# Kernel tuning notes

Hardware: AMD Instinct MI355X
Metric: run time of the kernel (lower is better)

## Reference

```python
import jax, jax.numpy as jnp
import numpy as np

B, T, C = 4, 2048, 1024
H, D = 16, 64  # n_head, head_dim; H*D == C
EPS = 1e-12


def _l2norm(x):
    # matches torch F.normalize(dim=-1): x / max(||x||_2, eps)
    n = jnp.sqrt(jnp.sum(x * x, axis=-1, keepdims=True))
    return x / jnp.maximum(n, EPS)


def setup_inputs() -> dict:
    key = jax.random.key(0)
    ks = jax.random.split(key, 8)
    s = 0.02
    return {
        "x": jax.random.normal(ks[0], (B, T, C), dtype=jnp.float32),
        "Wq": jax.random.normal(ks[1], (C, C), dtype=jnp.float32) * s,
        "Wk": jax.random.normal(ks[2], (C, C), dtype=jnp.float32) * s,
        "Wv": jax.random.normal(ks[3], (C, C), dtype=jnp.float32) * s,
        "Wbeta": jax.random.normal(ks[4], (H, C), dtype=jnp.float32) * s,
        "bbeta": jnp.zeros((H,), dtype=jnp.float32),
        "Wgate": jax.random.normal(ks[5], (C, C), dtype=jnp.float32) * s,
        "Wo": jax.random.normal(ks[6], (C, C), dtype=jnp.float32) * s,
    }


def _forward(x, Wq, Wk, Wv, Wbeta, bbeta, Wgate, Wo):
    q = (x @ Wq.T).reshape(B, T, H, D)
    k = (x @ Wk.T).reshape(B, T, H, D)
    v = (x @ Wv.T).reshape(B, T, H, D)
    beta = jax.nn.sigmoid(x @ Wbeta.T + bbeta)  # (B,T,H)
    gate = jax.nn.sigmoid(x @ Wgate.T)          # (B,T,C)

    q = _l2norm(q)
    k = _l2norm(k)

    # time-major for scan: (T,B,H,D) / (T,B,H)
    qT = jnp.transpose(q, (1, 0, 2, 3))
    kT = jnp.transpose(k, (1, 0, 2, 3))
    vT = jnp.transpose(v, (1, 0, 2, 3))
    bT = jnp.transpose(beta, (1, 0, 2))

    M0 = jnp.zeros((B, H, D, D), dtype=x.dtype)

    def step(M, inp):
        q_t, k_t, v_t, b_t = inp
        o_t = jnp.einsum('bhdc,bhc->bhd', M, q_t)       # read state with q (pre-update)
        Mk = jnp.einsum('bhdc,bhc->bhd', M, k_t)
        dv = v_t - Mk                                    # delta-rule error
        M = M + b_t[..., None, None] * jnp.einsum('bhd,bhc->bhdc', dv, k_t)
        return M, o_t

    _, oT = jax.lax.scan(step, M0, (qT, kT, vT, bT))     # oT: (T,B,H,D)
    o = jnp.transpose(oT, (1, 0, 2, 3)).reshape(B, T, C)
    return (gate * o) @ Wo.T


def reference(x, Wq, Wk, Wv, Wbeta, bbeta, Wgate, Wo):
    return _forward(x, Wq, Wk, Wv, Wbeta, bbeta, Wgate, Wo)
```

## Files before the change

### kernel.cpp

```cpp
#include <hip/hip_runtime.h>
#include <cstdint>
#include <cstddef>

#define Bz 4
#define Tz 2048
#define Cz 1024
#define Hz 16
#define Dz 64
#define NTOK (Bz*Tz)
#define CHL 32
#define NCH (Tz/CHL)

typedef __attribute__((ext_vector_type(8))) short  short8;
typedef __attribute__((ext_vector_type(4))) float  floatx4;

__device__ __forceinline__ unsigned short f2bf(float x) {
  union { float f; uint32_t u; } a; a.f = x;
  uint32_t r = a.u + 0x7fffu + ((a.u >> 16) & 1u);
  return (unsigned short)(r >> 16);
}
__device__ __forceinline__ float bf2f(unsigned short u) {
  union { uint32_t i; float f; } a; a.i = ((uint32_t)u) << 16; return a.f;
}
__device__ __forceinline__ float sigmoidf_(float z) {
  return 1.0f / (1.0f + __expf(-z));
}
__device__ __forceinline__ uint32_t cvtpk_bf16(float a, float b) {
  uint32_t d;
  asm volatile("v_cvt_pk_bf16_f32 %0, %1, %2" : "=v"(d) : "v"(a), "v"(b));
  return d;
}
__device__ __forceinline__ float lo16f(uint32_t u) {
  union { uint32_t i; float f; } a; a.i = u << 16; return a.f;
}
__device__ __forceinline__ float hi16f(uint32_t u) {
  union { uint32_t i; float f; } a; a.i = u & 0xffff0000u; return a.f;
}

__device__ __forceinline__ void gload_lds16(const void* gptr, void* lptr) {
  __builtin_amdgcn_global_load_lds(
      (const __attribute__((address_space(1))) void*)(uintptr_t)gptr,
      (__attribute__((address_space(3))) void*)(uint32_t)(uintptr_t)lptr,
      16, 0, 0);
}

template<int CTRL>
__device__ __forceinline__ float dpp_addf(float x) {
  int y = __builtin_amdgcn_update_dpp(0, __float_as_int(x), CTRL, 0xF, 0xF, true);
  return x + __int_as_float(y);
}
__device__ __forceinline__ float rowsum16(float x) {
  x = dpp_addf<0xB1>(x);
  x = dpp_addf<0x4E>(x);
  x = dpp_addf<0x124>(x);
  x = dpp_addf<0x128>(x);
  return x;
}

union FragU { uint32_t u[4]; short8 s; };

__global__ __launch_bounds__(256) void cvt6_kernel(
    const float* __restrict__ s0, const float* __restrict__ s1,
    const float* __restrict__ s2, const float* __restrict__ s3,
    const float* __restrict__ s4, const float* __restrict__ s5,
    unsigned short* __restrict__ d0, unsigned short* __restrict__ d1,
    unsigned short* __restrict__ d2, unsigned short* __restrict__ d3,
    unsigned short* __restrict__ d4, unsigned short* __restrict__ d5,
    int n4x, int n4w)
{
  const int w = blockIdx.y;
  const float* s = (w == 0) ? s0 : (w == 1) ? s1 : (w == 2) ? s2 : (w == 3) ? s3 : (w == 4) ? s4 : s5;
  unsigned short* d = (w == 0) ? d0 : (w == 1) ? d1 : (w == 2) ? d2 : (w == 3) ? d3 : (w == 4) ? d4 : d5;
  const int n4 = (w == 0) ? n4x : n4w;
  int i = blockIdx.x * blockDim.x + threadIdx.x;
  int stride = gridDim.x * blockDim.x;
  const float4* in4 = (const float4*)s;
  ushort4* out4 = (ushort4*)d;
  for (; i < n4; i += stride) {
    float4 f = in4[i];
    ushort4 u;
    u.x = f2bf(f.x); u.y = f2bf(f.y); u.z = f2bf(f.z); u.w = f2bf(f.w);
    out4[i] = u;
  }
}

#define VM8()  asm volatile("s_waitcnt vmcnt(8)" ::: "memory")
#define VM6()  asm volatile("s_waitcnt vmcnt(6)" ::: "memory")
#define VM4()  asm volatile("s_waitcnt vmcnt(4)" ::: "memory")
#define VM3()  asm volatile("s_waitcnt vmcnt(3)" ::: "memory")
#define VM0()  asm volatile("s_waitcnt vmcnt(0)" ::: "memory")
#define LGKM0() asm volatile("s_waitcnt lgkmcnt(0)" ::: "memory")
#define BARR() __builtin_amdgcn_s_barrier()

template<int BN, int OB16>
__global__ __launch_bounds__(512, 2) void gemm256_kernel(
    const unsigned short* __restrict__ A,
    const unsigned short* __restrict__ W0, const unsigned short* __restrict__ W1,
    const unsigned short* __restrict__ W2, const unsigned short* __restrict__ W3,
    void* __restrict__ O0, void* __restrict__ O1,
    void* __restrict__ O2, void* __restrict__ O3,
    int M, int N, int K, int nz_sigmoid, int norm_mask)
{
  constexpr int LB  = (BN == 256) ? 2 : 1;
  constexpr int NJ  = BN / 64;
  constexpr int AH  = 8192;
  constexpr int BH  = BN * 32;
  constexpr int PAR = 2 * AH + 2 * BH;
  __shared__ unsigned short smem[2 * PAR];

  const int gx = gridDim.x, gz = gridDim.z;
  const int nwg = gx * gridDim.y * gz;
  int flat = (blockIdx.z * gridDim.y + blockIdx.y) * gx + blockIdx.x;
  if ((nwg & 7) == 0) flat = (flat & 7) * (nwg >> 3) + (flat >> 3);
  const int xz = gx * gz;
  const int by = flat / xz;
  const int rem = flat - by * xz;
  const int bz = rem / gx;
  const int bx = rem - bz * gx;

  const unsigned short* Bw = (bz == 0) ? W0 : (bz == 1) ? W1 : (bz == 2) ? W2 : W3;
  void* Cw = (bz == 0) ? O0 : (bz == 1) ? O1 : (bz == 2) ? O2 : O3;
  const bool act = (bz == nz_sigmoid);
  const bool donorm = (norm_mask >> bz) & 1;

  const int m0 = by * 256, n0 = bx * BN;
  const int tid = threadIdx.x;
  const int wid = tid >> 6, lane = tid & 63;
  const int wm = wid >> 2, wn = wid & 3;
  const int ml = lane & 15, kq = lane >> 4;

  const unsigned short* Ap = A  + (size_t)m0 * K;
  const unsigned short* Bp = Bw + (size_t)n0 * K;

  const int srow = wid * 16 + (lane >> 2);
  const int ss8  = ((lane & 3) ^ ((lane >> 3) & 3)) * 8;
  const int rs8  = (kq ^ ((ml >> 1) & 3)) * 8;
  const int arow = wm * 128 + ml;
  const int brow = wn * (BN / 4) + ml;

  const int NT = K >> 6;
  const int hmax = NT << 2;

  floatx4 acc[8][NJ];
#pragma unroll
  for (int i = 0; i < 8; ++i)
#pragma unroll
    for (int j = 0; j < NJ; ++j) acc[i][j] = floatx4{0.f, 0.f, 0.f, 0.f};

#define HOFF(hh) ((hh) == 0 ? 0 : (hh) == 1 ? AH : (hh) == 2 ? AH + BH : 2 * AH + BH)
#define STAGE1(hsi) do {                                                      \
    const int ht_ = (hsi) >> 2, hh_ = (hsi) & 3;                              \
    const bool isB_ = hh_ & 1;                                                \
    const unsigned short* p_ = isB_ ? Bp : Ap;                                \
    const int kb_ = ht_ * 64 + (hh_ >> 1) * 32;                               \
    unsigned short* lb_ = &smem[(ht_ & 1) * PAR + HOFF(hh_) + wid * 512];     \
    gload_lds16(p_ + (size_t)srow * K + kb_ + ss8, lb_);                      \
    if (!isB_ || LB == 2)                                                     \
      gload_lds16(p_ + (size_t)(128 + srow) * K + kb_ + ss8, lb_ + 4096);     \
  } while (0)

  int hs = 0;
  for (; hs < 6 && hs < hmax; ++hs) STAGE1(hs);
  if constexpr (BN == 256) { VM8(); } else { VM6(); }
  BARR();

#define LOAD_A(Hb, mh)                                                        \
  _Pragma("unroll") for (int i = 0; i < 4; ++i)                               \
    af[i] = *(const short8*)&Hb[(arow + (mh) * 64 + i * 16) * 32 + rs8];
#define LOAD_B(Hb)                                                            \
  _Pragma("unroll") for (int j = 0; j < NJ; ++j)                              \
    bf[j] = *(const short8*)&Hb[(brow + j * 16) * 32 + rs8];
#define MFMA_Q(mh)                                                            \
  __builtin_amdgcn_s_setprio(1);                                              \
  _Pragma("unroll") for (int i = 0; i < 4; ++i)                               \
    _Pragma("unroll") for (int j = 0; j < NJ; ++j)                            \
      acc[(mh) * 4 + i][j] = __builtin_amdgcn_mfma_f32_16x16x32_bf16(         \
          af[i], bf[j], acc[(mh) * 4 + i][j], 0, 0, 0);                       \
  __builtin_amdgcn_s_setprio(0);
#define STAGE_NEXT() do { if (hs < hmax) { STAGE1(hs); ++hs; } } while (0)

  short8 af[4], bf[NJ];
  for (int t = 0; t < NT; ++t) {
    const unsigned short* Ah0 = &smem[(t & 1) * PAR + HOFF(0)];
    const unsigned short* Bh0 = &smem[(t & 1) * PAR + HOFF(1)];
    const unsigned short* Ah1 = &smem[(t & 1) * PAR + HOFF(2)];
    const unsigned short* Bh1 = &smem[(t & 1) * PAR + HOFF(3)];

    LOAD_A(Ah0, 0); LOAD_B(Bh0);
    STAGE_NEXT();
    BARR(); LGKM0();
    MFMA_Q(0);
    BARR();

    LOAD_A(Ah0, 1);
    STAGE_NEXT();
    BARR(); LGKM0();
    MFMA_Q(1);
    if (t == NT - 1) { VM0(); }
    else { if constexpr (BN == 256) { VM8(); } else { VM6(); } }
    BARR();

    LOAD_A(Ah1, 0); LOAD_B(Bh1);
    STAGE_NEXT();
    BARR(); LGKM0();
    MFMA_Q(0);
    BARR();

    LOAD_A(Ah1, 1);
    STAGE_NEXT();
    BARR(); LGKM0();
    MFMA_Q(1);
    if (t < NT - 2) { if constexpr (BN == 256) { VM8(); } else { VM6(); } }
    else if (t == NT - 2) { if constexpr (BN == 256) { VM4(); } else { VM3(); } }
    BARR();
  }

  float scale[8][4];
  if (donorm) {
#pragma unroll
    for (int i = 0; i < 8; ++i) {
#pragma unroll
      for (int r = 0; r < 4; ++r) {
        float ss = 0.f;
#pragma unroll
        for (int j = 0; j < NJ; ++j) ss = fmaf(acc[i][j][r], acc[i][j][r], ss);
        ss = rowsum16(ss);
        scale[i][r] = 1.0f / fmaxf(sqrtf(ss), 1e-12f);
      }
    }
  }

  const int row_base = m0 + wm * 128;
  const int col_base = n0 + wn * (BN / 4);
#pragma unroll
  for (int i = 0; i < 8; ++i) {
#pragma unroll
    for (int j = 0; j < NJ; ++j) {
      const int col = col_base + j * 16 + ml;
#pragma unroll
      for (int r = 0; r < 4; ++r) {
        const int row = row_base + i * 16 + kq * 4 + r;
        float val = acc[i][j][r];
        if (donorm) val *= scale[i][r];
        if (act) val = sigmoidf_(val);
        if constexpr (OB16) ((unsigned short*)Cw)[(size_t)row * N + col] = f2bf(val);
        else                ((float*)Cw)[(size_t)row * N + col] = val;
      }
    }
  }
}

__global__ __launch_bounds__(256) void beta_kernel(
    const float* __restrict__ x, const float* __restrict__ Wb,
    const float* __restrict__ bb, float* __restrict__ beta_out)
{
  const int n = blockIdx.x;
  const int wid = threadIdx.x >> 6;
  const int lane = threadIdx.x & 63;
  const float* xr = x + (size_t)n * Cz;
  for (int h = wid; h < Hz; h += 4) {
    const float* wr = Wb + (size_t)h * Cz;
    float s = 0.f;
#pragma unroll 4
    for (int i = lane; i < Cz; i += 64) s = fmaf(xr[i], wr[i], s);
#pragma unroll
    for (int ofs = 32; ofs >= 1; ofs >>= 1) s += __shfl_xor(s, ofs);
    if (lane == 0) beta_out[(size_t)n * Hz + h] = sigmoidf_(s + bb[h]);
  }
}

__global__ __launch_bounds__(256) void deltachunk_phase1(
    const unsigned short* __restrict__ qb, const unsigned short* __restrict__ kb,
    const unsigned short* __restrict__ vb, const float* __restrict__ betaf,
    float* __restrict__ of,
    unsigned short* __restrict__ qtb, unsigned short* __restrict__ wbuf,
    unsigned short* __restrict__ ubuf, unsigned short* __restrict__ ktb)
{
  __shared__ unsigned short Kb[32][72], Qb[32][72], Vb[32][72];
  __shared__ float As[32][36];
  __shared__ unsigned short Sb[32][40];
  __shared__ unsigned short Us[32][72], Ws[32][72], Qts[32][72];
  __shared__ float bsh[32];

  const int bid = blockIdx.x;
  const int chain = bid & 63;
  const int chunk = bid >> 6;
  const int b = chain >> 4, h = chain & 15;
  const int tid = threadIdx.x;
  const int wid = tid >> 6, lane = tid & 63;
  const int ml = lane & 15, kq = lane >> 4;

  const size_t tok0 = (size_t)b * Tz + (size_t)chunk * CHL;
  const size_t cb = ((size_t)chain * NCH + chunk) * 2048;

  {
    const int row = tid >> 3, c8 = (tid & 7) * 8;
    const size_t ga = (tok0 + row) * Cz + h * Dz + c8;
    *(uint4*)&Qb[row][c8] = *(const uint4*)&qb[ga];
    *(uint4*)&Kb[row][c8] = *(const uint4*)&kb[ga];
    *(uint4*)&Vb[row][c8] = *(const uint4*)&vb[ga];
  }
  if (tid < 32) bsh[tid] = betaf[(tok0 + tid) * Hz + h];
  __syncthreads();

  {
    const int tr = wid & 1, tc = wid >> 1;
    floatx4 accA = {0.f,0.f,0.f,0.f}, accS = {0.f,0.f,0.f,0.f};
#pragma unroll
    for (int eh = 0; eh < 2; ++eh) {
      short8 ka = *(const short8*)&Kb[tr * 16 + ml][eh * 32 + kq * 8];
      short8 kbf = *(const short8*)&Kb[tc * 16 + ml][eh * 32 + kq * 8];
      short8 qa = *(const short8*)&Qb[tr * 16 + ml][eh * 32 + kq * 8];
      accA = __builtin_amdgcn_mfma_f32_16x16x32_bf16(ka, kbf, accA, 0, 0, 0);
      accS = __builtin_amdgcn_mfma_f32_16x16x32_bf16(qa, kbf, accS, 0, 0, 0);
    }
#pragma unroll
    for (int r = 0; r < 4; ++r) {
      int t = tr * 16 + kq * 4 + r;
      int s = tc * 16 + ml;
      As[s][t] = bsh[t] * accA[r];
      Sb[t][s] = (t > s) ? f2bf(accS[r]) : (unsigned short)0;
    }
  }
  __syncthreads();

  if (tid < 128) {
    const int j = tid;
    float x[32];
    if (j < 64) {
#pragma unroll
      for (int t = 0; t < 32; ++t) x[t] = bsh[t] * bf2f(Vb[t][j]);
    } else {
#pragma unroll
      for (int t = 0; t < 32; ++t) x[t] = bsh[t] * bf2f(Kb[t][j - 64]);
    }
#pragma unroll
    for (int t = 0; t < 31; ++t) {
      float xt = x[t];
#pragma unroll
      for (int s = t + 1; s < 32; ++s) x[s] = fmaf(-As[t][s], xt, x[s]);
    }
    if (j < 64) {
#pragma unroll
      for (int t = 0; t < 32; ++t) Us[t][j] = f2bf(x[t]);
    } else {
#pragma unroll
      for (int t = 0; t < 32; ++t) Ws[t][j - 64] = f2bf(x[t]);
    }
  }
  __syncthreads();

  {
    const int dw = wid * 16 + ml;
    FragU bu, bw;
#pragma unroll
    for (int r = 0; r < 4; ++r) {
      bu.u[r] = (uint32_t)Us[kq * 8 + 2 * r][dw] | ((uint32_t)Us[kq * 8 + 2 * r + 1][dw] << 16);
      bw.u[r] = (uint32_t)Ws[kq * 8 + 2 * r][dw] | ((uint32_t)Ws[kq * 8 + 2 * r + 1][dw] << 16);
    }
    floatx4 accO[2], accQ[2];
#pragma unroll
    for (int tt = 0; tt < 2; ++tt) { accO[tt] = floatx4{0.f,0.f,0.f,0.f}; accQ[tt] = floatx4{0.f,0.f,0.f,0.f}; }
#pragma unroll
    for (int tt = 0; tt < 2; ++tt) {
      short8 sa = *(const short8*)&Sb[tt * 16 + ml][kq * 8];
      accO[tt] = __builtin_amdgcn_mfma_f32_16x16x32_bf16(sa, bu.s, accO[tt], 0, 0, 0);
      accQ[tt] = __builtin_amdgcn_mfma_f32_16x16x32_bf16(sa, bw.s, accQ[tt], 0, 0, 0);
    }
#pragma unroll
    for (int tt = 0; tt < 2; ++tt) {
#pragma unroll
      for (int r = 0; r < 4; ++r) {
        int t = tt * 16 + kq * 4 + r;
        of[(tok0 + t) * Cz + h * Dz + dw] = accO[tt][r];
        Qts[t][dw] = f2bf(bf2f(Qb[t][dw]) - accQ[tt][r]);
      }
    }
  }

  unsigned short ktmp[8], utmp[8];
  {
    const int e = tid >> 2, tq = (tid & 3) * 8;
#pragma unroll
    for (int i2 = 0; i2 < 8; ++i2) { ktmp[i2] = Kb[tq + i2][e]; utmp[i2] = Us[tq + i2][e]; }
  }
  __syncthreads();

  {
    const int row = tid >> 3, c8 = (tid & 7) * 8;
    const size_t o16 = cb + (size_t)row * 64 + c8;
    *(uint4*)&qtb[o16]  = *(const uint4*)&Qts[row][c8];
    *(uint4*)&wbuf[o16] = *(const uint4*)&Ws[row][c8];
    const int e = tid >> 2, tq = (tid & 3) * 8;
    *(uint4*)&ktb[cb + (size_t)e * 32 + tq]  = *(const uint4*)ktmp;
    *(uint4*)&ubuf[cb + (size_t)e * 32 + tq] = *(const uint4*)utmp;
  }
}

__global__ __launch_bounds__(256) void deltachunk_phase2(
    const unsigned short* __restrict__ qtb, const unsigned short* __restrict__ wbuf,
    const unsigned short* __restrict__ ubuf, const unsigned short* __restrict__ ktb,
    const unsigned short* __restrict__ gbuf, const float* __restrict__ ofv,
    unsigned short* __restrict__ ab)
{
  __shared__ unsigned short Gb[2][64][72];
  __shared__ unsigned short Ub[2][32][40];
  __shared__ unsigned short Kts[2][64][40];
  __shared__ unsigned short Mh[2][32][72], Ml[2][32][72];

  const int chain = blockIdx.x >> 1;
  const int dh = blockIdx.x & 1;
  const int b = chain >> 4, h = chain & 15;
  const int d0 = dh * 32;
  const int tid = threadIdx.x;
  const int wid = tid >> 6, lane = tid & 63;
  const int ml = lane & 15, kq = lane >> 4;
  const int iq = wid >> 1, jq = wid & 1;

  const size_t cbase = (size_t)chain * NCH * 2048;
  const int gcol = h * Dz + d0 + jq * 16 + ml;

  const int grow = tid >> 2;
  const int gc16 = (tid & 3) * 16;
  const int ke   = tid >> 2;
  const int kc8  = (tid & 3) * 8;
  const int ue   = tid >> 3;
  const int uc4  = (tid & 7) * 4;

  const unsigned short* gsrc = (grow < 32) ? qtb : wbuf;
  const size_t gsoff = (size_t)(grow & 31) * 64 + gc16;

  unsigned short pg[8]; float pf[8];
  {
    *(uint4*)&Gb[0][grow][gc16]     = *(const uint4*)&gsrc[cbase + gsoff];
    *(uint4*)&Gb[0][grow][gc16 + 8] = *(const uint4*)&gsrc[cbase + gsoff + 8];
    *(uint4*)&Kts[0][ke][kc8]       = *(const uint4*)&ktb[cbase + (size_t)ke * 32 + kc8];
    *(uint2*)&Ub[0][ue][uc4]        = *(const uint2*)&ubuf[cbase + (size_t)(d0 + ue) * 32 + uc4];
  }
  if (iq == 0) {
    const size_t t0 = (size_t)b * Tz;
#pragma unroll
    for (int ti = 0; ti < 2; ++ti)
#pragma unroll
      for (int r = 0; r < 4; ++r) {
        const size_t gi = (t0 + ti * 16 + kq * 4 + r) * Cz + gcol;
        pg[ti * 4 + r] = gbuf[gi];
        pf[ti * 4 + r] = ofv[gi];
      }
  }
  for (int i = tid; i < 32 * 72; i += 256) { (&Mh[0][0][0])[i] = 0; (&Ml[0][0][0])[i] = 0; }
  __syncthreads();

  const int idxA = (ml + 16 * ((kq & 1) * 2)) * 4;
  const int idxB = (ml + 16 * ((kq & 1) * 2 + 1)) * 4;
  const bool hiKq = (kq >= 2);

  floatx4 mAcc[4];
#pragma unroll
  for (int a = 0; a < 4; ++a) mAcc[a] = floatx4{0.f, 0.f, 0.f, 0.f};

  for (int c = 0; c < NCH; ++c) {
    const int cbuf = c & 1, nbuf = cbuf ^ 1;
    const int mr = c & 1, mw = mr ^ 1;
    const size_t tok0 = (size_t)b * Tz + (size_t)c * CHL;

    const int cn = (c + 1 < NCH) ? c + 1 : c;
    const size_t cbn = cbase + (size_t)cn * 2048;
    uint4 sg0 = *(const uint4*)&gsrc[cbn + gsoff];
    uint4 sg1 = *(const uint4*)&gsrc[cbn + gsoff + 8];
    uint4 sk  = *(const uint4*)&ktb[cbn + (size_t)ke * 32 + kc8];
    uint2 su  = *(const uint2*)&ubuf[cbn + (size_t)(d0 + ue) * 32 + uc4];
    unsigned short ng[8]; float nf[8];
    if (iq == 0) {
      const size_t tkn = (size_t)b * Tz + (size_t)cn * CHL;
#pragma unroll
      for (int ti = 0; ti < 2; ++ti)
#pragma unroll
        for (int r = 0; r < 4; ++r) {
          const size_t gi = (tkn + ti * 16 + kq * 4 + r) * Cz + gcol;
          ng[ti * 4 + r] = gbuf[gi];
          nf[ti * 4 + r] = ofv[gi];
        }
    }

    floatx4 g1[2];
    g1[0] = floatx4{0.f,0.f,0.f,0.f}; g1[1] = floatx4{0.f,0.f,0.f,0.f};
#pragma unroll
    for (int eh = 0; eh < 2; ++eh) {
      short8 afr0 = *(const short8*)&Gb[cbuf][iq * 32 + 0  + ml][eh * 32 + kq * 8];
      short8 afr1 = *(const short8*)&Gb[cbuf][iq * 32 + 16 + ml][eh * 32 + kq * 8];
      short8 bh = *(const short8*)&Mh[mr][jq * 16 + ml][eh * 32 + kq * 8];
      short8 bl = *(const short8*)&Ml[mr][jq * 16 + ml][eh * 32 + kq * 8];
      g1[0] = __builtin_amdgcn_mfma_f32_16x16x32_bf16(afr0, bh, g1[0], 0, 0, 0);
      g1[0] = __builtin_amdgcn_mfma_f32_16x16x32_bf16(afr0, bl, g1[0], 0, 0, 0);
      g1[1] = __builtin_amdgcn_mfma_f32_16x16x32_bf16(afr1, bh, g1[1], 0, 0, 0);
      g1[1] = __builtin_amdgcn_mfma_f32_16x16x32_bf16(afr1, bl, g1[1], 0, 0, 0);
    }

    if (iq == 0) {
#pragma unroll
      for (int ti = 0; ti < 2; ++ti)
#pragma unroll
        for (int r = 0; r < 4; ++r) {
          const size_t gi = (tok0 + ti * 16 + kq * 4 + r) * Cz + gcol;
          const float val = bf2f(pg[ti * 4 + r]) * (pf[ti * 4 + r] + g1[ti][r]);
          ab[gi] = f2bf(val);
        }
#pragma unroll
      for (int e = 0; e < 8; ++e) { pg[e] = ng[e]; pf[e] = nf[e]; }
    } else {
      uint32_t pkh[2][2], pkl[2][2];
#pragma unroll
      for (int ti = 0; ti < 2; ++ti) {
        ushort4 uu = *(const ushort4*)&Ub[cbuf][jq * 16 + ml][ti * 16 + kq * 4];
        float z0 = bf2f(uu.x) - g1[ti][0];
        float z1 = bf2f(uu.y) - g1[ti][1];
        float z2 = bf2f(uu.z) - g1[ti][2];
        float z3 = bf2f(uu.w) - g1[ti][3];
        uint32_t h01 = cvtpk_bf16(z0, z1), h23 = cvtpk_bf16(z2, z3);
        pkh[ti][0] = h01; pkh[ti][1] = h23;
        pkl[ti][0] = cvtpk_bf16(z0 - lo16f(h01), z1 - hi16f(h01));
        pkl[ti][1] = cvtpk_bf16(z2 - lo16f(h23), z3 - hi16f(h23));
      }
      FragU zh, zl;
#pragma unroll
      for (int s = 0; s < 4; ++s) {
        const int idx = (s < 2) ? idxA : idxB;
        const int rp = s & 1;
        int v0 = __builtin_amdgcn_ds_bpermute(idx, (int)pkh[0][rp]);
        int v1 = __builtin_amdgcn_ds_bpermute(idx, (int)pkh[1][rp]);
        zh.u[s] = hiKq ? (uint32_t)v1 : (uint32_t)v0;
        int w0 = __builtin_amdgcn_ds_bpermute(idx, (int)pkl[0][rp]);
        int w1 = __builtin_amdgcn_ds_bpermute(idx, (int)pkl[1][rp]);
        zl.u[s] = hiKq ? (uint32_t)w1 : (uint32_t)w0;
      }
#pragma unroll
      for (int et = 0; et < 4; ++et) {
        short8 kfr = *(const short8*)&Kts[cbuf][et * 16 + ml][kq * 8];
        mAcc[et] = __builtin_amdgcn_mfma_f32_16x16x32_bf16(kfr, zh.s, mAcc[et], 0, 0, 0);
        mAcc[et] = __builtin_amdgcn_mfma_f32_16x16x32_bf16(kfr, zl.s, mAcc[et], 0, 0, 0);
      }
#pragma unroll
      for (int et = 0; et < 4; ++et) {
        float m0 = mAcc[et][0], m1 = mAcc[et][1], m2 = mAcc[et][2], m3 = mAcc[et][3];
        uint32_t h01 = cvtpk_bf16(m0, m1), h23 = cvtpk_bf16(m2, m3);
        uint32_t l01 = cvtpk_bf16(m0 - lo16f(h01), m1 - hi16f(h01));
        uint32_t l23 = cvtpk_bf16(m2 - lo16f(h23), m3 - hi16f(h23));
        *(uint2*)&Mh[mw][jq * 16 + ml][et * 16 + kq * 4] = make_uint2(h01, h23);
        *(uint2*)&Ml[mw][jq * 16 + ml][et * 16 + kq * 4] = make_uint2(l01, l23);
      }
    }

    *(uint4*)&Gb[nbuf][grow][gc16]     = sg0;
    *(uint4*)&Gb[nbuf][grow][gc16 + 8] = sg1;
    *(uint4*)&Kts[nbuf][ke][kc8]       = sk;
    *(uint2*)&Ub[nbuf][ue][uc4]        = su;

    LGKM0();
    BARR();
  }
}

extern "C" void kernel_launch(void* const* d_in, const int* in_sizes, int n_in,
                              void* d_out, int out_size, void* d_ws, size_t ws_size,
                              hipStream_t stream) {
  const float* x     = (const float*)d_in[0];
  const float* Wq    = (const float*)d_in[1];
  const float* Wk    = (const float*)d_in[2];
  const float* Wv    = (const float*)d_in[3];
  const float* Wbeta = (const float*)d_in[4];
  const float* bbeta = (const float*)d_in[5];
  const float* Wgate = (const float*)d_in[6];
  const float* Wo    = (const float*)d_in[7];
  float* out = (float*)d_out;

  char* ws = (char*)d_ws;
  size_t off = 0;
  auto alloc = [&](size_t bytes) -> char* {
    char* p = ws + off;
    off += (bytes + 255) & ~(size_t)255;
    return p;
  };
  unsigned short* xb  = (unsigned short*)alloc((size_t)NTOK * Cz * 2);
  unsigned short* Wqb = (unsigned short*)alloc((size_t)Cz * Cz * 2);
  unsigned short* Wkb = (unsigned short*)alloc((size_t)Cz * Cz * 2);
  unsigned short* Wvb = (unsigned short*)alloc((size_t)Cz * Cz * 2);
  unsigned short* Wgb = (unsigned short*)alloc((size_t)Cz * Cz * 2);
  unsigned short* Wob = (unsigned short*)alloc((size_t)Cz * Cz * 2);
  unsigned short* qb  = (unsigned short*)alloc((size_t)NTOK * Cz * 2);
  unsigned short* kb  = (unsigned short*)alloc((size_t)NTOK * Cz * 2);
  unsigned short* vb  = (unsigned short*)alloc((size_t)NTOK * Cz * 2);
  unsigned short* gb  = (unsigned short*)alloc((size_t)NTOK * Cz * 2);
  float* of    = (float*)alloc((size_t)NTOK * Cz * 4);
  float* betaf = (float*)alloc((size_t)NTOK * Hz * 4);
  unsigned short* qtb  = (unsigned short*)alloc((size_t)64 * NCH * 2048 * 2);
  unsigned short* wbuf = (unsigned short*)alloc((size_t)64 * NCH * 2048 * 2);
  unsigned short* ubuf = (unsigned short*)alloc((size_t)64 * NCH * 2048 * 2);
  unsigned short* ktb  = (unsigned short*)alloc((size_t)64 * NCH * 2048 * 2);
  unsigned short* ab = xb;

  const int n4x = NTOK * Cz / 4;
  const int n4w = Cz * Cz / 4;

  cvt6_kernel<<<dim3(1024, 6), dim3(256), 0, stream>>>(
      x, Wq, Wk, Wv, Wgate, Wo, xb, Wqb, Wkb, Wvb, Wgb, Wob, n4x, n4w);

  gemm256_kernel<256, 1><<<dim3(Cz / 256, NTOK / 256, 4), dim3(512), 0, stream>>>(
      xb, Wqb, Wkb, Wvb, Wgb, qb, kb, vb, gb, NTOK, Cz, Cz, 3, 3);

  beta_kernel<<<dim3(NTOK), dim3(256), 0, stream>>>(x, Wbeta, bbeta, betaf);

  deltachunk_phase1<<<dim3(64 * NCH), dim3(256), 0, stream>>>(
      qb, kb, vb, betaf, of, qtb, wbuf, ubuf, ktb);

  deltachunk_phase2<<<dim3(128), dim3(256), 0, stream>>>(
      qtb, wbuf, ubuf, ktb, gb, of, ab);

  gemm256_kernel<128, 0><<<dim3(Cz / 128, NTOK / 256, 1), dim3(512), 0, stream>>>(
      ab, Wob, Wob, Wob, Wob, out, out, out, out, NTOK, Cz, Cz, -1, 0);
}
```

Before: 366.9 us.

## Fuse x bf16 conversion into beta kernel and merge phase2 halves per block

```diff
diff --git a/kernel.cpp b/kernel.cpp
--- a/kernel.cpp
+++ b/kernel.cpp
@@ -59,28 +59,23 @@
 
 union FragU { uint32_t u[4]; short8 s; };
 
-__global__ __launch_bounds__(256) void cvt6_kernel(
+__global__ __launch_bounds__(256) void cvt5_kernel(
     const float* __restrict__ s0, const float* __restrict__ s1,
     const float* __restrict__ s2, const float* __restrict__ s3,
-    const float* __restrict__ s4, const float* __restrict__ s5,
+    const float* __restrict__ s4,
     unsigned short* __restrict__ d0, unsigned short* __restrict__ d1,
     unsigned short* __restrict__ d2, unsigned short* __restrict__ d3,
-    unsigned short* __restrict__ d4, unsigned short* __restrict__ d5,
-    int n4x, int n4w)
+    unsigned short* __restrict__ d4, int n4)
 {
   const int w = blockIdx.y;
-  const float* s = (w == 0) ? s0 : (w == 1) ? s1 : (w == 2) ? s2 : (w == 3) ? s3 : (w == 4) ? s4 : s5;
-  unsigned short* d = (w == 0) ? d0 : (w == 1) ? d1 : (w == 2) ? d2 : (w == 3) ? d3 : (w == 4) ? d4 : d5;
-  const int n4 = (w == 0) ? n4x : n4w;
+  const float* s = (w == 0) ? s0 : (w == 1) ? s1 : (w == 2) ? s2 : (w == 3) ? s3 : s4;
+  unsigned short* d = (w == 0) ? d0 : (w == 1) ? d1 : (w == 2) ? d2 : (w == 3) ? d3 : d4;
   int i = blockIdx.x * blockDim.x + threadIdx.x;
-  int stride = gridDim.x * blockDim.x;
-  const float4* in4 = (const float4*)s;
-  ushort4* out4 = (ushort4*)d;
-  for (; i < n4; i += stride) {
-    float4 f = in4[i];
+  if (i < n4) {
+    float4 f = ((const float4*)s)[i];
     ushort4 u;
     u.x = f2bf(f.x); u.y = f2bf(f.y); u.z = f2bf(f.z); u.w = f2bf(f.w);
-    out4[i] = u;
+    ((ushort4*)d)[i] = u;
   }
 }
 
@@ -252,12 +247,19 @@
 
 __global__ __launch_bounds__(256) void beta_kernel(
     const float* __restrict__ x, const float* __restrict__ Wb,
-    const float* __restrict__ bb, float* __restrict__ beta_out)
+    const float* __restrict__ bb, float* __restrict__ beta_out,
+    unsigned short* __restrict__ xb16)
 {
   const int n = blockIdx.x;
   const int wid = threadIdx.x >> 6;
   const int lane = threadIdx.x & 63;
   const float* xr = x + (size_t)n * Cz;
+  {
+    float4 f = ((const float4*)xr)[threadIdx.x];
+    ushort4 u;
+    u.x = f2bf(f.x); u.y = f2bf(f.y); u.z = f2bf(f.z); u.w = f2bf(f.w);
+    ((ushort4*)(xb16 + (size_t)n * Cz))[threadIdx.x] = u;
+  }
   for (int h = wid; h < Hz; h += 4) {
     const float* wr = Wb + (size_t)h * Cz;
     float s = 0.f;
@@ -397,45 +399,41 @@
   }
 }
 
-__global__ __launch_bounds__(256) void deltachunk_phase2(
+__global__ __launch_bounds__(512) void deltachunk_phase2(
     const unsigned short* __restrict__ qtb, const unsigned short* __restrict__ wbuf,
     const unsigned short* __restrict__ ubuf, const unsigned short* __restrict__ ktb,
     const unsigned short* __restrict__ gbuf, const float* __restrict__ ofv,
     unsigned short* __restrict__ ab)
 {
   __shared__ unsigned short Gb[2][64][72];
-  __shared__ unsigned short Ub[2][32][40];
+  __shared__ unsigned short Ub[2][64][40];
   __shared__ unsigned short Kts[2][64][40];
-  __shared__ unsigned short Mh[2][32][72], Ml[2][32][72];
-
-  const int chain = blockIdx.x >> 1;
-  const int dh = blockIdx.x & 1;
+  __shared__ unsigned short Mh[2][2][32][72], Ml[2][2][32][72];
+
+  const int chain = blockIdx.x;
   const int b = chain >> 4, h = chain & 15;
-  const int d0 = dh * 32;
   const int tid = threadIdx.x;
   const int wid = tid >> 6, lane = tid & 63;
   const int ml = lane & 15, kq = lane >> 4;
-  const int iq = wid >> 1, jq = wid & 1;
+  const int dh = wid >> 2;
+  const int iq = (wid >> 1) & 1, jq = wid & 1;
+  const int d0 = dh * 32;
 
   const size_t cbase = (size_t)chain * NCH * 2048;
   const int gcol = h * Dz + d0 + jq * 16 + ml;
 
-  const int grow = tid >> 2;
-  const int gc16 = (tid & 3) * 16;
-  const int ke   = tid >> 2;
-  const int kc8  = (tid & 3) * 8;
-  const int ue   = tid >> 3;
-  const int uc4  = (tid & 7) * 4;
+  const int grow = tid >> 3, gc8 = (tid & 7) * 8;
+  const int ke   = tid >> 3, kc4 = (tid & 7) * 4;
+  const int ue   = tid >> 3, uc4 = (tid & 7) * 4;
 
   const unsigned short* gsrc = (grow < 32) ? qtb : wbuf;
-  const size_t gsoff = (size_t)(grow & 31) * 64 + gc16;
+  const size_t gsoff = (size_t)(grow & 31) * 64 + gc8;
 
   unsigned short pg[8]; float pf[8];
   {
-    *(uint4*)&Gb[0][grow][gc16]     = *(const uint4*)&gsrc[cbase + gsoff];
-    *(uint4*)&Gb[0][grow][gc16 + 8] = *(const uint4*)&gsrc[cbase + gsoff + 8];
-    *(uint4*)&Kts[0][ke][kc8]       = *(const uint4*)&ktb[cbase + (size_t)ke * 32 + kc8];
-    *(uint2*)&Ub[0][ue][uc4]        = *(const uint2*)&ubuf[cbase + (size_t)(d0 + ue) * 32 + uc4];
+    *(uint4*)&Gb[0][grow][gc8] = *(const uint4*)&gsrc[cbase + gsoff];
+    *(uint2*)&Kts[0][ke][kc4]  = *(const uint2*)&ktb[cbase + (size_t)ke * 32 + kc4];
+    *(uint2*)&Ub[0][ue][uc4]   = *(const uint2*)&ubuf[cbase + (size_t)ue * 32 + uc4];
   }
   if (iq == 0) {
     const size_t t0 = (size_t)b * Tz;
@@ -448,7 +446,7 @@
         pf[ti * 4 + r] = ofv[gi];
       }
   }
-  for (int i = tid; i < 32 * 72; i += 256) { (&Mh[0][0][0])[i] = 0; (&Ml[0][0][0])[i] = 0; }
+  for (int i = tid; i < 2 * 32 * 72; i += 512) { (&Mh[0][0][0][0])[i] = 0; (&Ml[0][0][0][0])[i] = 0; }
   __syncthreads();
 
   const int idxA = (ml + 16 * ((kq & 1) * 2)) * 4;
@@ -466,10 +464,9 @@
 
     const int cn = (c + 1 < NCH) ? c + 1 : c;
     const size_t cbn = cbase + (size_t)cn * 2048;
-    uint4 sg0 = *(const uint4*)&gsrc[cbn + gsoff];
-    uint4 sg1 = *(const uint4*)&gsrc[cbn + gsoff + 8];
-    uint4 sk  = *(const uint4*)&ktb[cbn + (size_t)ke * 32 + kc8];
-    uint2 su  = *(const uint2*)&ubuf[cbn + (size_t)(d0 + ue) * 32 + uc4];
+    uint4 sg = *(const uint4*)&gsrc[cbn + gsoff];
+    uint2 sk = *(const uint2*)&ktb[cbn + (size_t)ke * 32 + kc4];
+    uint2 su = *(const uint2*)&ubuf[cbn + (size_t)ue * 32 + uc4];
     unsigned short ng[8]; float nf[8];
     if (iq == 0) {
       const size_t tkn = (size_t)b * Tz + (size_t)cn * CHL;
@@ -489,8 +486,8 @@
     for (int eh = 0; eh < 2; ++eh) {
       short8 afr0 = *(const short8*)&Gb[cbuf][iq * 32 + 0  + ml][eh * 32 + kq * 8];
       short8 afr1 = *(const short8*)&Gb[cbuf][iq * 32 + 16 + ml][eh * 32 + kq * 8];
-      short8 bh = *(const short8*)&Mh[mr][jq * 16 + ml][eh * 32 + kq * 8];
-      short8 bl = *(const short8*)&Ml[mr][jq * 16 + ml][eh * 32 + kq * 8];
+      short8 bh = *(const short8*)&Mh[mr][dh][jq * 16 + ml][eh * 32 + kq * 8];
+      short8 bl = *(const short8*)&Ml[mr][dh][jq * 16 + ml][eh * 32 + kq * 8];
       g1[0] = __builtin_amdgcn_mfma_f32_16x16x32_bf16(afr0, bh, g1[0], 0, 0, 0);
       g1[0] = __builtin_amdgcn_mfma_f32_16x16x32_bf16(afr0, bl, g1[0], 0, 0, 0);
       g1[1] = __builtin_amdgcn_mfma_f32_16x16x32_bf16(afr1, bh, g1[1], 0, 0, 0);
@@ -512,7 +509,7 @@
       uint32_t pkh[2][2], pkl[2][2];
 #pragma unroll
       for (int ti = 0; ti < 2; ++ti) {
-        ushort4 uu = *(const ushort4*)&Ub[cbuf][jq * 16 + ml][ti * 16 + kq * 4];
+        ushort4 uu = *(const ushort4*)&Ub[cbuf][d0 + jq * 16 + ml][ti * 16 + kq * 4];
         float z0 = bf2f(uu.x) - g1[ti][0];
         float z1 = bf2f(uu.y) - g1[ti][1];
         float z2 = bf2f(uu.z) - g1[ti][2];
@@ -546,15 +543,14 @@
         uint32_t h01 = cvtpk_bf16(m0, m1), h23 = cvtpk_bf16(m2, m3);
         uint32_t l01 = cvtpk_bf16(m0 - lo16f(h01), m1 - hi16f(h01));
         uint32_t l23 = cvtpk_bf16(m2 - lo16f(h23), m3 - hi16f(h23));
-        *(uint2*)&Mh[mw][jq * 16 + ml][et * 16 + kq * 4] = make_uint2(h01, h23);
-        *(uint2*)&Ml[mw][jq * 16 + ml][et * 16 + kq * 4] = make_uint2(l01, l23);
-      }
-    }
-
-    *(uint4*)&Gb[nbuf][grow][gc16]     = sg0;
-    *(uint4*)&Gb[nbuf][grow][gc16 + 8] = sg1;
-    *(uint4*)&Kts[nbuf][ke][kc8]       = sk;
-    *(uint2*)&Ub[nbuf][ue][uc4]        = su;
+        *(uint2*)&Mh[mw][dh][jq * 16 + ml][et * 16 + kq * 4] = make_uint2(h01, h23);
+        *(uint2*)&Ml[mw][dh][jq * 16 + ml][et * 16 + kq * 4] = make_uint2(l01, l23);
+      }
+    }
+
+    *(uint4*)&Gb[nbuf][grow][gc8] = sg;
+    *(uint2*)&Kts[nbuf][ke][kc4]  = sk;
+    *(uint2*)&Ub[nbuf][ue][uc4]   = su;
 
     LGKM0();
     BARR();
@@ -602,18 +598,18 @@
   const int n4x = NTOK * Cz / 4;
   const int n4w = Cz * Cz / 4;
 
-  cvt6_kernel<<<dim3(1024, 6), dim3(256), 0, stream>>>(
-      x, Wq, Wk, Wv, Wgate, Wo, xb, Wqb, Wkb, Wvb, Wgb, Wob, n4x, n4w);
+  cvt5_kernel<<<dim3(n4w / 256, 5), dim3(256), 0, stream>>>(
+      Wq, Wk, Wv, Wgate, Wo, Wqb, Wkb, Wvb, Wgb, Wob, n4w);
+
+  beta_kernel<<<dim3(NTOK), dim3(256), 0, stream>>>(x, Wbeta, bbeta, betaf, xb);
 
   gemm256_kernel<256, 1><<<dim3(Cz / 256, NTOK / 256, 4), dim3(512), 0, stream>>>(
       xb, Wqb, Wkb, Wvb, Wgb, qb, kb, vb, gb, NTOK, Cz, Cz, 3, 3);
 
-  beta_kernel<<<dim3(NTOK), dim3(256), 0, stream>>>(x, Wbeta, bbeta, betaf);
-
   deltachunk_phase1<<<dim3(64 * NCH), dim3(256), 0, stream>>>(
       qb, kb, vb, betaf, of, qtb, wbuf, ubuf, ktb);
 
-  deltachunk_phase2<<<dim3(128), dim3(256), 0, stream>>>(
+  deltachunk_phase2<<<dim3(64), dim3(512), 0, stream>>>(
       qtb, wbuf, ubuf, ktb, gb, of, ab);
 
   gemm256_kernel<128, 0><<<dim3(Cz / 128, NTOK / 256, 1), dim3(512), 0, stream>>>(
```

Result: slower. 378.4 us (+3.1%).
